# Performance work log

Measured on AMD Instinct MI355X. Metric: run time of the kernel, lower is better.

Reference implementation:

```python
import jax, jax.numpy as jnp
import numpy as np
import math

GRID_SIZE = 5
ORDER = 3
TAU = 0.1            # HuxleyRD tau (constructor default)
Q_SCALE = 64 / 2.0   # SaturatedQuantizer levels=64


def make_grid():
    h = 2.0 / GRID_SIZE
    # knots: arange(-order, grid_size+order+1)*h - 1  -> 12 values, shared by all in_features
    return jnp.arange(-ORDER, GRID_SIZE + ORDER + 1, dtype=jnp.float32) * h - 1.0


def b_splines(x, grid):
    # x: [b, in] -> bases: [b, in, GRID_SIZE+ORDER] via vectorized Cox-de Boor
    xg = x[..., None]
    g = grid  # [12], identical per feature so plain broadcasting suffices
    bases = ((xg >= g[:-1]) & (xg < g[1:])).astype(x.dtype)  # [b, in, 11]
    for p in range(1, ORDER + 1):
        t_i, t_ip = g[:-1 - p], g[p:-1]
        term1 = (xg - t_i) / (t_ip - t_i + 1e-8) * bases[..., :-1]
        t_i1, t_ip1 = g[1:-p], g[p + 1:]
        term2 = (t_ip1 - xg) / (t_ip1 - t_i1 + 1e-8) * bases[..., 1:]
        bases = term1 + term2
    return bases  # [b, in, 8]


def kan_layer(x, base_w, spline_w, grid):
    base = x @ base_w.T
    basis = b_splines(x, grid)
    # SaturatedQuantizer forward (round to levels); STE expressed via stop_gradient
    qw = spline_w + jax.lax.stop_gradient(jnp.round(spline_w * Q_SCALE) / Q_SCALE - spline_w)
    return base + jnp.einsum('bic,oic->bo', basis, qw)


def trig_unfolding(u, gcve_pressure, chirality, tau_decay):
    # u: [b, n]
    tr_c = jnp.sum(u * u, axis=-1)                                   # [b]
    uf_abs = jnp.abs(jnp.fft.rfft(u, axis=-1))                       # [b, n//2+1]
    det_pas = jnp.var(uf_abs, axis=-1, ddof=1) + 1e-6                # torch.var is unbiased
    denom = 2.0 * jnp.sqrt(det_pas) ** 3 + 1e-8
    cos_3phi = jnp.clip((3.0 * gcve_pressure - tr_c / tau_decay) / denom, -0.999, 0.999)
    phi = jnp.arccos(cos_3phi) / 3.0                                 # [b]
    lam_min = jnp.min(uf_abs, axis=-1)                               # [b]
    amp = 2.0 * jnp.sqrt(lam_min / 3.0 + 1e-8)                       # [b]
    ks = jnp.arange(3, dtype=u.dtype)                                # branch indices 0,1,2
    cos_terms = jnp.cos(phi[None, :] + 2.0 * jnp.pi * ks[:, None] / 3.0)   # [3, b]
    shifts = jnp.exp(-jnp.abs(chirality)[None, :] * ks[:, None])           # [3, b]
    coef = amp[None, :] * cos_terms * shifts                                # [3, b]
    branches = coef[:, :, None] * u[None, :, :]                             # [3, b, n]
    energies = jnp.linalg.norm(branches, axis=-1)                           # [3, b]
    best_k = jnp.argmax(energies, axis=0)                                   # [b]
    mask = (best_k[None, :] == jnp.arange(3)[:, None]).astype(u.dtype)      # [3, b]
    return jnp.sum(branches * mask[:, :, None], axis=0)


def huxley_rd(u, spectral_gate, kernel, a, gamma, tau_decay, soliton_velocity,
              gcve_pressure, chirality):
    N = u.shape[-1]
    # HarmonicWaveDecomposition: spectral sigmoid gate split
    uf = jnp.fft.rfft(u, axis=-1)
    gate = jax.nn.sigmoid(spectral_gate)
    u_erg = jnp.fft.irfft(uf * gate, n=N, axis=-1)
    u_ne = jnp.fft.irfft(uf * (1.0 - gate), n=N, axis=-1)
    # ergodic: cubic reaction + 3-tap diffusion conv (padding=1, cross-correlation)
    reaction = u_erg * (u_erg - a) * (1.0 - u_erg)
    up = jnp.pad(u_erg, ((0, 0), (1, 1)))
    diffusion = kernel[0] * up[:, :-2] + kernel[1] * up[:, 1:-1] + kernel[2] * up[:, 2:]
    u_erg_next = u_erg + TAU * (reaction + gamma * diffusion)
    # non-ergodic: spectral phase shift (soliton translation)
    nef = jnp.fft.rfft(u_ne, axis=-1)
    k_idx = jnp.arange(nef.shape[-1], dtype=jnp.float32)
    phase = jnp.exp(-1j * 2.0 * jnp.pi * k_idx * soliton_velocity / N)
    u_ne_shift = jnp.fft.irfft(nef * phase, n=N, axis=-1)
    u_ne_unf = trig_unfolding(u_ne_shift, gcve_pressure, chirality, tau_decay)
    s = u_erg_next + u_ne_unf
    return jax.nn.sigmoid(s) * s  # SiLU-style fusion


def setup_inputs() -> dict:
    key = jax.random.key(0)
    ks = jax.random.split(key, 12)
    B, NIN, W, NOUT = 4096, 512, 1024, 1024
    return {
        'c': jax.random.uniform(ks[0], (B, NIN), jnp.float32, -1.0, 1.0),
        'base_w0': jax.random.normal(ks[1], (W, NIN), jnp.float32) * (1.0 / np.sqrt(NIN)),
        'spline_w0': jax.random.normal(ks[2], (W, NIN, 8), jnp.float32) * 0.1,
        'base_w1': jax.random.normal(ks[3], (W, W), jnp.float32) * (1.0 / np.sqrt(W)),
        'spline_w1': jax.random.normal(ks[4], (W, W, 8), jnp.float32) * 0.1,
        'base_w2': jax.random.normal(ks[5], (NOUT, W), jnp.float32) * (1.0 / np.sqrt(W)),
        'spline_w2': jax.random.normal(ks[6], (NOUT, W, 8), jnp.float32) * 0.1,
        'spectral_gate': jnp.ones((NOUT // 2 + 1,), jnp.float32),
        'diffusion_kernel': jnp.asarray([0.1, -0.2, 0.1], jnp.float32),
        'a_param': jnp.asarray(0.1, jnp.float32),
        'gamma': jnp.asarray(1.0, jnp.float32),
        'tau_decay': jnp.asarray(0.1, jnp.float32),
        'soliton_velocity': jnp.asarray(0.25, jnp.float32),
        'gcve_pressure': jax.random.uniform(ks[7], (B,), jnp.float32),
        'chirality': jax.random.normal(ks[8], (B,), jnp.float32),
    }


def reference(c, base_w0, spline_w0, base_w1, spline_w1, base_w2, spline_w2,
              spectral_gate, diffusion_kernel, a_param, gamma, tau_decay,
              soliton_velocity, gcve_pressure, chirality):
    grid = make_grid()
    x = kan_layer(c, base_w0, spline_w0, grid)
    x = kan_layer(x, base_w1, spline_w1, grid)
    x = kan_layer(x, base_w2, spline_w2, grid)
    return huxley_rd(x, spectral_gate, diffusion_kernel, a_param, gamma,
                     tau_decay, soliton_velocity, gcve_pressure, chirality)
```

## Files before the change

kernel.cpp:

```cpp
#include <hip/hip_runtime.h>
#include <math.h>

typedef _Float16 f16;
typedef _Float16 f16x8 __attribute__((ext_vector_type(8)));
typedef float f32x4 __attribute__((ext_vector_type(4)));

__global__ __launch_bounds__(256) void expand_sum_a(
    const float* __restrict__ src, size_t plane, int Sin,
    f16* __restrict__ Aexp, int KIN, int shift)
{
    int idx = blockIdx.x * 256 + threadIdx.x;
    int i = idx & (KIN - 1);
    int b = idx >> shift;
    float x = 0.0f;
    for (int s = 0; s < Sin; ++s) x += src[(size_t)s * plane + idx];

    float xs = (x + 2.2f) * 2.5f;
    float fj = floorf(xs);
    int jj = (int)fj;
    float t = xs - fj;
    float t2 = t * t, t3 = t2 * t;
    float omt = 1.0f - t;
    float p0 = omt * omt * omt * (1.0f / 6.0f);
    float p1 = (3.0f * t3 - 6.0f * t2 + 4.0f) * (1.0f / 6.0f);
    float p2 = (-3.0f * t3 + 3.0f * t2 + 3.0f * t + 1.0f) * (1.0f / 6.0f);
    float p3 = t3 * (1.0f / 6.0f);

    union { f16 h[8]; uint4 v; } hi, lo;
    bool inr = (jj >= 0 && jj <= 10);
    #pragma unroll
    for (int cc = 0; cc < 8; ++cc) {
        int d = cc - (jj - 3);
        float v = 0.0f;
        if (inr) {
            if (d == 0) v = p0; else if (d == 1) v = p1;
            else if (d == 2) v = p2; else if (d == 3) v = p3;
        }
        f16 h = (f16)v;
        hi.h[cc] = h;
        lo.h[cc] = (f16)(v - (float)h);
    }
    size_t KEXP = (size_t)KIN * 19;
    f16* row = Aexp + (size_t)b * KEXP;
    *(uint4*)(row + (size_t)i * 8) = hi.v;
    *(uint4*)(row + (size_t)KIN * 8 + (size_t)i * 8) = lo.v;
    f16 xh = (f16)x;
    f16 xl = (f16)(x - (float)xh);
    int K16 = KIN * 16;
    row[K16 + i] = xh;
    row[K16 + KIN + i] = xh;
    row[K16 + 2 * KIN + i] = xl;
}

__global__ __launch_bounds__(256) void prep_b(
    const float* __restrict__ BW, const float* __restrict__ SW,
    f16* __restrict__ Bexp, int KIN, int shift)
{
    int idx = blockIdx.x * 256 + threadIdx.x;
    int i = idx & (KIN - 1);
    int o = idx >> shift;
    const float* sp = SW + ((size_t)o * KIN + i) * 8;
    union { f16 h[8]; uint4 v; } pk;
    #pragma unroll
    for (int cc = 0; cc < 8; ++cc)
        pk.h[cc] = (f16)(rintf(sp[cc] * 32.0f) * 0.03125f);
    size_t KEXP = (size_t)KIN * 19;
    f16* row = Bexp + (size_t)o * KEXP;
    *(uint4*)(row + (size_t)i * 8) = pk.v;
    *(uint4*)(row + (size_t)KIN * 8 + (size_t)i * 8) = pk.v;
    float w = BW[(size_t)o * KIN + i];
    f16 wh = (f16)w;
    f16 wl = (f16)(w - (float)wh);
    int K16 = KIN * 16;
    row[K16 + i] = wh;
    row[K16 + KIN + i] = wl;
    row[K16 + 2 * KIN + i] = wh;
}

__global__ __launch_bounds__(512, 2) void gemm_mfma(
    const f16* __restrict__ A, const f16* __restrict__ Bm,
    float* __restrict__ C, int Kfull, int Kc, size_t plane, int N)
{
    __shared__ __align__(16) f16 As[4][8192];
    __shared__ __align__(16) f16 Bs[4][8192];

    const int tid = threadIdx.x;
    const int wave = tid >> 6, lane = tid & 63;

    const int nwg = gridDim.x * gridDim.y * gridDim.z;
    const int b = blockIdx.x + gridDim.x * (blockIdx.y + gridDim.y * blockIdx.z);
    const int q = nwg >> 3;
    const int L = (b & 7) * q + (b >> 3);
    const int lx = L % gridDim.x;
    const int rest = L / gridDim.x;
    const int ly = rest % gridDim.y;
    const int lz = rest / gridDim.y;

    const int m0 = ly * 256, n0 = lx * 256;
    const int kb = lz * Kc;
    int kcl = Kfull - kb; if (kcl > Kc) kcl = Kc;
    const int NT = kcl >> 5;

    const int kc_src = (lane & 3) ^ ((lane >> 3) & 3);
    const f16* gb[4];
    int isA_[4], coff[4];
    #pragma unroll
    for (int j = 0; j < 4; ++j) {
        int cch = wave * 4 + j;
        int a = (cch < 16);
        int c8 = a ? cch : (cch - 16);
        int row0 = (a ? m0 : n0) + c8 * 16 + (lane >> 2);
        gb[j] = (a ? A : Bm) + (size_t)row0 * Kfull + kb + kc_src * 8;
        isA_[j] = a;
        coff[j] = c8 * 512;
    }

    f32x4 acc[8][4];
    #pragma unroll
    for (int i = 0; i < 8; ++i)
        #pragma unroll
        for (int j = 0; j < 4; ++j)
            acc[i][j] = (f32x4){0.f, 0.f, 0.f, 0.f};

    #pragma unroll
    for (int s = 0; s < 3; ++s) {
        if (s < NT) {
            int k0 = s << 5;
            #pragma unroll
            for (int j = 0; j < 4; ++j) {
                f16* dp = isA_[j] ? &As[s][coff[j]] : &Bs[s][coff[j]];
                __builtin_amdgcn_global_load_lds(
                    (const __attribute__((address_space(1))) unsigned int*)(gb[j] + k0),
                    (__attribute__((address_space(3))) unsigned int*)dp, 16, 0, 0);
            }
        }
    }
    if (NT >= 3)      asm volatile("s_waitcnt vmcnt(8)" ::: "memory");
    else if (NT == 2) asm volatile("s_waitcnt vmcnt(4)" ::: "memory");
    else              asm volatile("s_waitcnt vmcnt(0)" ::: "memory");
    __builtin_amdgcn_s_barrier();
    asm volatile("" ::: "memory");

    const int lr = lane & 15;
    const int ko = (((lane >> 4) ^ ((lr >> 1) & 3)) & 3) * 8;
    const int wm = (wave & 1) * 128, wn = (wave >> 1) * 64;

    for (int t = 0; t < NT; ++t) {
        const int st = t & 3;
        const int ns = (t + 3) & 3;
        const bool pf = (t + 3 < NT);
        const int kn = (t + 3) << 5;
        const int rem = NT - 1 - t;

        f16x8 af[4], bf[4], ag[4];
        #pragma unroll
        for (int i = 0; i < 4; ++i)
            af[i] = *(const f16x8*)&As[st][(wm + i * 16 + lr) * 32 + ko];
        #pragma unroll
        for (int j = 0; j < 4; ++j)
            bf[j] = *(const f16x8*)&Bs[st][(wn + j * 16 + lr) * 32 + ko];
        __builtin_amdgcn_sched_barrier(0);
        #pragma unroll
        for (int i = 0; i < 4; ++i)
            ag[i] = *(const f16x8*)&As[st][(wm + 64 + i * 16 + lr) * 32 + ko];
        __builtin_amdgcn_sched_barrier(0);

        if (rem >= 2)      asm volatile("s_waitcnt vmcnt(4)" ::: "memory");
        else if (rem == 1) asm volatile("s_waitcnt vmcnt(0)" ::: "memory");
        if (rem >= 1) {
            __builtin_amdgcn_s_barrier();
            asm volatile("" ::: "memory");
        }

        if (pf) {
            #pragma unroll
            for (int j = 0; j < 4; ++j) {
                f16* dp = isA_[j] ? &As[ns][coff[j]] : &Bs[ns][coff[j]];
                __builtin_amdgcn_global_load_lds(
                    (const __attribute__((address_space(1))) unsigned int*)(gb[j] + kn),
                    (__attribute__((address_space(3))) unsigned int*)dp, 16, 0, 0);
            }
        }

        asm volatile("s_waitcnt lgkmcnt(4)" ::: "memory");
        __builtin_amdgcn_sched_barrier(0);
        __builtin_amdgcn_s_setprio(1);
        #pragma unroll
        for (int i = 0; i < 4; ++i)
            #pragma unroll
            for (int j = 0; j < 4; ++j)
                acc[i][j] = __builtin_amdgcn_mfma_f32_16x16x32_f16(af[i], bf[j], acc[i][j], 0, 0, 0);
        __builtin_amdgcn_s_setprio(0);

        asm volatile("s_waitcnt lgkmcnt(0)" ::: "memory");
        __builtin_amdgcn_sched_barrier(0);
        __builtin_amdgcn_s_setprio(1);
        #pragma unroll
        for (int i = 0; i < 4; ++i)
            #pragma unroll
            for (int j = 0; j < 4; ++j)
                acc[4 + i][j] = __builtin_amdgcn_mfma_f32_16x16x32_f16(ag[i], bf[j], acc[4 + i][j], 0, 0, 0);
        __builtin_amdgcn_s_setprio(0);
    }

    float* Cp = C + (size_t)lz * plane;
    #pragma unroll
    for (int i = 0; i < 8; ++i) {
        int row = m0 + wm + i * 16 + (lane >> 4) * 4;
        #pragma unroll
        for (int j = 0; j < 4; ++j) {
            int col = n0 + wn + j * 16 + lr;
            #pragma unroll
            for (int rr = 0; rr < 4; ++rr)
                Cp[(size_t)(row + rr) * N + col] = acc[i][j][rr];
        }
    }
}

__global__ __launch_bounds__(256) void kan_gemm(
    const float* __restrict__ X, const float* __restrict__ BW,
    const float* __restrict__ SW, float* __restrict__ Y, int KIN, int OUT)
{
    __shared__ __align__(16) float Asf[72][68];
    __shared__ __align__(16) float Bsf[72][68];
    const int tid = threadIdx.x;
    const int n0 = blockIdx.x * 64;
    const int m0 = blockIdx.y * 64;
    const int tx = tid & 15;
    const int ty = tid >> 4;
    float acc[4][4] = {};
    for (int k0 = 0; k0 < KIN; k0 += 8) {
        #pragma unroll
        for (int rep = 0; rep < 2; ++rep) {
            int idx = rep * 256 + tid;
            int r = idx >> 3, c = idx & 7;
            float x = X[(size_t)(m0 + r) * KIN + k0 + c];
            int bk = c * 9;
            Asf[bk][r] = x;
            #pragma unroll
            for (int z = 0; z < 8; ++z) Asf[bk + 1 + z][r] = 0.0f;
            float xs = (x + 2.2f) * 2.5f;
            float fj = floorf(xs);
            int j = (int)fj;
            if (j >= 0 && j <= 10) {
                float t = xs - fj;
                float t2 = t * t, t3 = t2 * t;
                float omt = 1.0f - t;
                float p0 = omt * omt * omt * (1.0f / 6.0f);
                float p1 = (3.0f * t3 - 6.0f * t2 + 4.0f) * (1.0f / 6.0f);
                float p2 = (-3.0f * t3 + 3.0f * t2 + 3.0f * t + 1.0f) * (1.0f / 6.0f);
                float p3 = t3 * (1.0f / 6.0f);
                if (j >= 3) Asf[bk + 1 + j - 3][r] = p0;
                if (j >= 2 && j <= 9) Asf[bk + 1 + j - 2][r] = p1;
                if (j >= 1 && j <= 8) Asf[bk + 1 + j - 1][r] = p2;
                if (j <= 7) Asf[bk + 1 + j][r] = p3;
            }
        }
        #pragma unroll
        for (int rep = 0; rep < 16; ++rep) {
            int idx = rep * 256 + tid;
            int ol = idx >> 6;
            int l = idx & 63;
            int i = l >> 3, cc = l & 7;
            float v = SW[((size_t)(n0 + ol) * KIN + k0 + i) * 8 + cc];
            Bsf[i * 9 + 1 + cc][ol] = rintf(v * 32.0f) * 0.03125f;
        }
        #pragma unroll
        for (int rep = 0; rep < 2; ++rep) {
            int idx = rep * 256 + tid;
            int ol = idx >> 3, cc = idx & 7;
            Bsf[cc * 9][ol] = BW[(size_t)(n0 + ol) * KIN + k0 + cc];
        }
        __syncthreads();
        #pragma unroll 8
        for (int kk = 0; kk < 72; ++kk) {
            float4 av = *(const float4*)&Asf[kk][ty * 4];
            float4 bv = *(const float4*)&Bsf[kk][tx * 4];
            acc[0][0] += av.x * bv.x; acc[0][1] += av.x * bv.y; acc[0][2] += av.x * bv.z; acc[0][3] += av.x * bv.w;
            acc[1][0] += av.y * bv.x; acc[1][1] += av.y * bv.y; acc[1][2] += av.y * bv.z; acc[1][3] += av.y * bv.w;
            acc[2][0] += av.z * bv.x; acc[2][1] += av.z * bv.y; acc[2][2] += av.z * bv.z; acc[2][3] += av.z * bv.w;
            acc[3][0] += av.w * bv.x; acc[3][1] += av.w * bv.y; acc[3][2] += av.w * bv.z; acc[3][3] += av.w * bv.w;
        }
        __syncthreads();
    }
    #pragma unroll
    for (int i = 0; i < 4; ++i) {
        float4 o = make_float4(acc[i][0], acc[i][1], acc[i][2], acc[i][3]);
        *(float4*)&Y[(size_t)(m0 + ty * 4 + i) * OUT + n0 + tx * 4] = o;
    }
}

__device__ __forceinline__ float block_reduce_sum(float v, float* red, int tid) {
    red[tid] = v; __syncthreads();
    #pragma unroll
    for (int s = 128; s > 0; s >>= 1) {
        if (tid < s) red[tid] += red[tid + s];
        __syncthreads();
    }
    float r = red[0]; __syncthreads();
    return r;
}
__device__ __forceinline__ float block_reduce_min(float v, float* red, int tid) {
    red[tid] = v; __syncthreads();
    #pragma unroll
    for (int s = 128; s > 0; s >>= 1) {
        if (tid < s) red[tid] = fminf(red[tid], red[tid + s]);
        __syncthreads();
    }
    float r = red[0]; __syncthreads();
    return r;
}

__device__ void fft1024(float2* X, const float2* tw, int tid, bool inverse) {
    if (!inverse) {
        for (int sh = 9; sh >= 0; --sh) {
            int h = 1 << sh;
            #pragma unroll
            for (int q = 0; q < 2; ++q) {
                int b = tid + q * 256;
                int g = b >> sh, j = b & (h - 1);
                int i0 = (g << (sh + 1)) + j, i1 = i0 + h;
                float2 u = X[i0], v = X[i1];
                float dx = u.x - v.x, dy = u.y - v.y;
                X[i0] = make_float2(u.x + v.x, u.y + v.y);
                float2 w = tw[j << (9 - sh)];
                X[i1] = make_float2(dx * w.x + dy * w.y, dy * w.x - dx * w.y);
            }
            __syncthreads();
        }
    } else {
        for (int sh = 0; sh <= 9; ++sh) {
            int h = 1 << sh;
            #pragma unroll
            for (int q = 0; q < 2; ++q) {
                int b = tid + q * 256;
                int g = b >> sh, j = b & (h - 1);
                int i0 = (g << (sh + 1)) + j, i1 = i0 + h;
                float2 u = X[i0], v = X[i1];
                float2 w = tw[j << (9 - sh)];
                float tx2 = v.x * w.x - v.y * w.y;
                float ty2 = v.x * w.y + v.y * w.x;
                X[i0] = make_float2(u.x + tx2, u.y + ty2);
                X[i1] = make_float2(u.x - tx2, u.y - ty2);
            }
            __syncthreads();
        }
    }
}

__global__ __launch_bounds__(256) void huxley_kernel(
    const float* __restrict__ Pin, size_t plane, int S,
    float* __restrict__ dst,
    const float* __restrict__ sg, const float* __restrict__ dk,
    const float* __restrict__ pa, const float* __restrict__ pgam,
    const float* __restrict__ ptau, const float* __restrict__ pvel,
    const float* __restrict__ gp, const float* __restrict__ chi)
{
    __shared__ float2 A[1024];
    __shared__ float2 Bb[1024];
    __shared__ float sErg[1024];
    __shared__ float sAbs[516];
    __shared__ float2 tw[512];
    __shared__ float red[256];
    __shared__ float sG[516];

    const int tid = threadIdx.x;
    const int row = blockIdx.x;
    const float* pin = Pin + (size_t)row * 1024;
    float* uo = dst + (size_t)row * 1024;

    for (int m = tid; m < 512; m += 256) {
        float s, c;
        sincosf(6.283185307179586f * (float)m * (1.0f / 1024.0f), &s, &c);
        tw[m] = make_float2(c, s);
    }
    for (int k = tid; k < 513; k += 256)
        sG[k] = 1.0f / (1.0f + expf(-sg[k]));
    for (int i = tid; i < 1024; i += 256) {
        float s = 0.0f;
        for (int ss = 0; ss < S; ++ss) s += pin[(size_t)ss * plane + i];
        A[i] = make_float2(s, 0.0f);
    }
    __syncthreads();

    fft1024(A, tw, tid, false);

    for (int p = tid; p < 1024; p += 256) {
        int k = (int)(__brev((unsigned)p) >> 22);
        int m = (k <= 512) ? k : 1024 - k;
        float g = sG[m] * (1.0f / 1024.0f);
        Bb[p] = make_float2(A[p].x * g, A[p].y * g);
    }
    __syncthreads();
    fft1024(Bb, tw, tid, true);
    for (int i = tid; i < 1024; i += 256) sErg[i] = Bb[i].x;
    __syncthreads();

    const float vv = pvel[0];
    for (int p = tid; p < 1024; p += 256) {
        int k = (int)(__brev((unsigned)p) >> 22);
        int m = (k <= 512) ? k : 1024 - k;
        float omg = 1.0f - sG[m];
        float nx = A[p].x * omg, ny = A[p].y * omg;
        float ang = (k <= 512)
            ? (-6.283185307179586f * vv * (float)k * (1.0f / 1024.0f))
            : (6.283185307179586f * vv * (float)(1024 - k) * (1.0f / 1024.0f));
        float sn, cs;
        sincosf(ang, &sn, &cs);
        float yx = nx * cs - ny * sn;
        float yy = nx * sn + ny * cs;
        if (k < 512)       sAbs[k]   = sqrtf(nx * nx + ny * ny);
        else if (k == 512) sAbs[512] = fabsf(yx);
        Bb[p] = make_float2(yx * (1.0f / 1024.0f), yy * (1.0f / 1024.0f));
    }
    __syncthreads();
    fft1024(Bb, tw, tid, true);

    float loc = 0.0f;
    for (int i = tid; i < 1024; i += 256) { float x = Bb[i].x; loc += x * x; }
    float trc = block_reduce_sum(loc, red, tid);

    loc = 0.0f;
    for (int k = tid; k < 513; k += 256) loc += sAbs[k];
    float mean = block_reduce_sum(loc, red, tid) * (1.0f / 513.0f);

    loc = 0.0f;
    for (int k = tid; k < 513; k += 256) { float d = sAbs[k] - mean; loc += d * d; }
    float varsum = block_reduce_sum(loc, red, tid);

    loc = 3.4e38f;
    for (int k = tid; k < 513; k += 256) loc = fminf(loc, sAbs[k]);
    float lmin = block_reduce_min(loc, red, tid);

    float det_pas = varsum * (1.0f / 512.0f) + 1e-6f;
    float sd = sqrtf(det_pas);
    float denom = 2.0f * sd * sd * sd + 1e-8f;
    float c3 = (3.0f * gp[row] - trc / ptau[0]) / denom;
    c3 = fminf(fmaxf(c3, -0.999f), 0.999f);
    float ph = acosf(c3) * (1.0f / 3.0f);
    float amp = 2.0f * sqrtf(lmin * (1.0f / 3.0f) + 1e-8f);
    float nu = sqrtf(trc);
    float achi = fabsf(chi[row]);
    float cbest = 0.0f, ebest = -1.0f;
    #pragma unroll
    for (int kb = 0; kb < 3; ++kb) {
        float ck = amp * cosf(ph + 2.0943951023931953f * (float)kb) * expf(-achi * (float)kb);
        float ek = fabsf(ck) * nu;
        if (ek > ebest) { ebest = ek; cbest = ck; }
    }

    const float a = pa[0], gm = pgam[0];
    const float k0 = dk[0], k1 = dk[1], k2 = dk[2];
    for (int i = tid; i < 1024; i += 256) {
        float e = sErg[i];
        float l = (i > 0) ? sErg[i - 1] : 0.0f;
        float r = (i < 1023) ? sErg[i + 1] : 0.0f;
        float reac = e * (e - a) * (1.0f - e);
        float diff = k0 * l + k1 * e + k2 * r;
        float un = e + 0.1f * (reac + gm * diff);
        float s = un + cbest * Bb[i].x;
        uo[i] = s / (1.0f + expf(-s));
    }
}


extern "C" void kernel_launch(void* const* d_in, const int* in_sizes, int n_in,
                              void* d_out, int out_size, void* d_ws, size_t ws_size,
                              hipStream_t stream) {
    const float* c    = (const float*)d_in[0];
    const float* bw0  = (const float*)d_in[1];
    const float* sw0  = (const float*)d_in[2];
    const float* bw1  = (const float*)d_in[3];
    const float* sw1  = (const float*)d_in[4];
    const float* bw2  = (const float*)d_in[5];
    const float* sw2  = (const float*)d_in[6];
    const float* sg   = (const float*)d_in[7];
    const float* dk   = (const float*)d_in[8];
    const float* pa   = (const float*)d_in[9];
    const float* pgam = (const float*)d_in[10];
    const float* ptau = (const float*)d_in[11];
    const float* pvel = (const float*)d_in[12];
    const float* gp   = (const float*)d_in[13];
    const float* chi  = (const float*)d_in[14];

    const int B = 4096, NIN = 512, W = 1024, NOUT = 1024;
    const int KE0 = 19 * NIN, KE1 = 19 * W;
    const size_t MN = (size_t)B * W;
    const size_t BE = (size_t)W * KE1 * 2;
    dim3 blk(256);
    dim3 gblk(512);

    struct Cand { int CH, S; };
    const Cand cands[] = {
        {4096, 4}, {4096, 3}, {2048, 4}, {2048, 3}, {1024, 4},
        {512, 4}, {256, 4}
    };
    int CH = 0, S = 1;
    for (const auto& cd : cands) {
        size_t need = BE + (size_t)cd.CH * KE1 * 2 + (size_t)cd.S * MN * 4;
        if (need <= ws_size) { CH = cd.CH; S = cd.S; break; }
    }

    if (CH > 0) {
        f16* Bexp = (f16*)d_ws;
        float* P  = (float*)((char*)d_ws + BE);
        f16* Aexp = (f16*)((char*)d_ws + BE + (size_t)S * MN * 4);

        const int Kc0 = ((KE0 / 32 + S - 1) / S) * 32;
        const int Kc1 = ((KE1 / 32 + S - 1) / S) * 32;

        prep_b<<<(W * NIN) / 256, blk, 0, stream>>>(bw0, sw0, Bexp, NIN, 9);
        for (int r0 = 0; r0 < B; r0 += CH) {
            expand_sum_a<<<(CH * NIN) / 256, blk, 0, stream>>>(
                c + (size_t)r0 * NIN, 0, 1, Aexp, NIN, 9);
            gemm_mfma<<<dim3(W / 256, CH / 256, S), gblk, 0, stream>>>(
                Aexp, Bexp, P + (size_t)r0 * W, KE0, Kc0, MN, W);
        }
        prep_b<<<(W * W) / 256, blk, 0, stream>>>(bw1, sw1, Bexp, W, 10);
        for (int r0 = 0; r0 < B; r0 += CH) {
            expand_sum_a<<<(CH * W) / 256, blk, 0, stream>>>(
                P + (size_t)r0 * W, MN, S, Aexp, W, 10);
            gemm_mfma<<<dim3(W / 256, CH / 256, S), gblk, 0, stream>>>(
                Aexp, Bexp, P + (size_t)r0 * W, KE1, Kc1, MN, W);
        }
        prep_b<<<(NOUT * W) / 256, blk, 0, stream>>>(bw2, sw2, Bexp, W, 10);
        for (int r0 = 0; r0 < B; r0 += CH) {
            expand_sum_a<<<(CH * W) / 256, blk, 0, stream>>>(
                P + (size_t)r0 * W, MN, S, Aexp, W, 10);
            gemm_mfma<<<dim3(NOUT / 256, CH / 256, S), gblk, 0, stream>>>(
                Aexp, Bexp, P + (size_t)r0 * W, KE1, Kc1, MN, NOUT);
        }
        huxley_kernel<<<B, blk, 0, stream>>>(P, MN, S, (float*)d_out,
                                             sg, dk, pa, pgam, ptau, pvel, gp, chi);
    } else {
        float* fx0 = (float*)d_ws;
        float* fx1 = fx0 + (size_t)B * W;
        dim3 g0(W / 64, B / 64);
        kan_gemm<<<g0, blk, 0, stream>>>(c,   bw0, sw0, fx0, NIN, W);
        kan_gemm<<<g0, blk, 0, stream>>>(fx0, bw1, sw1, fx1, W,   W);
        dim3 g2(NOUT / 64, B / 64);
        kan_gemm<<<g2, blk, 0, stream>>>(fx1, bw2, sw2, (float*)d_out, W, NOUT);
        huxley_kernel<<<B, blk, 0, stream>>>((float*)d_out, 0, 1, (float*)d_out,
                                             sg, dk, pa, pgam, ptau, pvel, gp, chi);
    }
}
```

Before: 698.5 us.

## Switch MFMA GEMM to 64-wide K tiles with double-buffered LDS pipeline

Changes the GEMM main loop from a 4-stage ring of 32-wide K tiles to a 2-stage double buffer of 64-wide K tiles, with a new 8-way XOR swizzle. LDS fragment reads for the second K half are interleaved with the MFMAs of the first half, and the global-to-LDS prefetch is split in two halves. The aim is to halve the number of barriers per unit of K and overlap LDS reads with MFMA work. In exchange the prefetch distance drops to one stage, so global latency is less hidden, and the K-split chunk sizes must now be multiples of 64.

After: 690.8 us. Within noise of the previous version (-1.1%).

```diff
diff --git a/kernel.cpp b/kernel.cpp
--- a/kernel.cpp
+++ b/kernel.cpp
@@ -81,8 +81,8 @@
     const f16* __restrict__ A, const f16* __restrict__ Bm,
     float* __restrict__ C, int Kfull, int Kc, size_t plane, int N)
 {
-    __shared__ __align__(16) f16 As[4][8192];
-    __shared__ __align__(16) f16 Bs[4][8192];
+    __shared__ __align__(16) f16 As[2][16384];
+    __shared__ __align__(16) f16 Bs[2][16384];
 
     const int tid = threadIdx.x;
     const int wave = tid >> 6, lane = tid & 63;
@@ -99,17 +99,17 @@
     const int m0 = ly * 256, n0 = lx * 256;
     const int kb = lz * Kc;
     int kcl = Kfull - kb; if (kcl > Kc) kcl = Kc;
-    const int NT = kcl >> 5;
-
-    const int kc_src = (lane & 3) ^ ((lane >> 3) & 3);
-    const f16* gb[4];
-    int isA_[4], coff[4];
-    #pragma unroll
-    for (int j = 0; j < 4; ++j) {
-        int cch = wave * 4 + j;
-        int a = (cch < 16);
-        int c8 = a ? cch : (cch - 16);
-        int row0 = (a ? m0 : n0) + c8 * 16 + (lane >> 2);
+    const int NT = kcl >> 6;
+
+    const int kc_src = (lane & 7) ^ ((lane >> 3) & 7);
+    const f16* gb[8];
+    int isA_[8], coff[8];
+    #pragma unroll
+    for (int j = 0; j < 8; ++j) {
+        int cch = wave * 8 + j;
+        int a = (cch < 32);
+        int c8 = a ? cch : (cch - 32);
+        int row0 = (a ? m0 : n0) + c8 * 8 + (lane >> 3);
         gb[j] = (a ? A : Bm) + (size_t)row0 * Kfull + kb + kc_src * 8;
         isA_[j] = a;
         coff[j] = c8 * 512;
@@ -123,61 +123,47 @@
             acc[i][j] = (f32x4){0.f, 0.f, 0.f, 0.f};
 
     #pragma unroll
-    for (int s = 0; s < 3; ++s) {
-        if (s < NT) {
-            int k0 = s << 5;
-            #pragma unroll
-            for (int j = 0; j < 4; ++j) {
-                f16* dp = isA_[j] ? &As[s][coff[j]] : &Bs[s][coff[j]];
-                __builtin_amdgcn_global_load_lds(
-                    (const __attribute__((address_space(1))) unsigned int*)(gb[j] + k0),
-                    (__attribute__((address_space(3))) unsigned int*)dp, 16, 0, 0);
-            }
-        }
-    }
-    if (NT >= 3)      asm volatile("s_waitcnt vmcnt(8)" ::: "memory");
-    else if (NT == 2) asm volatile("s_waitcnt vmcnt(4)" ::: "memory");
-    else              asm volatile("s_waitcnt vmcnt(0)" ::: "memory");
+    for (int j = 0; j < 8; ++j) {
+        f16* dp = isA_[j] ? &As[0][coff[j]] : &Bs[0][coff[j]];
+        __builtin_amdgcn_global_load_lds(
+            (const __attribute__((address_space(1))) unsigned int*)(gb[j]),
+            (__attribute__((address_space(3))) unsigned int*)dp, 16, 0, 0);
+    }
+    asm volatile("s_waitcnt vmcnt(0)" ::: "memory");
     __builtin_amdgcn_s_barrier();
     asm volatile("" ::: "memory");
 
     const int lr = lane & 15;
-    const int ko = (((lane >> 4) ^ ((lr >> 1) & 3)) & 3) * 8;
+    const int g4 = lane >> 4;
+    const int ko0 = ((g4     ^ (lr & 7))) * 8;
+    const int ko1 = (((4|g4) ^ (lr & 7))) * 8;
     const int wm = (wave & 1) * 128, wn = (wave >> 1) * 64;
 
     for (int t = 0; t < NT; ++t) {
-        const int st = t & 3;
-        const int ns = (t + 3) & 3;
-        const bool pf = (t + 3 < NT);
-        const int kn = (t + 3) << 5;
-        const int rem = NT - 1 - t;
-
-        f16x8 af[4], bf[4], ag[4];
-        #pragma unroll
-        for (int i = 0; i < 4; ++i)
-            af[i] = *(const f16x8*)&As[st][(wm + i * 16 + lr) * 32 + ko];
+        const int st = t & 1;
+        const int ns = st ^ 1;
+        const bool pf = (t + 1 < NT);
+        const int kt = (t + 1) << 6;
+
+        f16x8 af0[4], bf0[4], ag0[4], af1[4], bf1[4], ag1[4];
+
+        #pragma unroll
+        for (int i = 0; i < 4; ++i)
+            af0[i] = *(const f16x8*)&As[st][(wm + i * 16 + lr) * 64 + ko0];
         #pragma unroll
         for (int j = 0; j < 4; ++j)
-            bf[j] = *(const f16x8*)&Bs[st][(wn + j * 16 + lr) * 32 + ko];
-        __builtin_amdgcn_sched_barrier(0);
-        #pragma unroll
-        for (int i = 0; i < 4; ++i)
-            ag[i] = *(const f16x8*)&As[st][(wm + 64 + i * 16 + lr) * 32 + ko];
-        __builtin_amdgcn_sched_barrier(0);
-
-        if (rem >= 2)      asm volatile("s_waitcnt vmcnt(4)" ::: "memory");
-        else if (rem == 1) asm volatile("s_waitcnt vmcnt(0)" ::: "memory");
-        if (rem >= 1) {
-            __builtin_amdgcn_s_barrier();
-            asm volatile("" ::: "memory");
-        }
-
+            bf0[j] = *(const f16x8*)&Bs[st][(wn + j * 16 + lr) * 64 + ko0];
+        __builtin_amdgcn_sched_barrier(0);
+        #pragma unroll
+        for (int i = 0; i < 4; ++i)
+            ag0[i] = *(const f16x8*)&As[st][(wm + 64 + i * 16 + lr) * 64 + ko0];
+        __builtin_amdgcn_sched_barrier(0);
         if (pf) {
             #pragma unroll
             for (int j = 0; j < 4; ++j) {
                 f16* dp = isA_[j] ? &As[ns][coff[j]] : &Bs[ns][coff[j]];
                 __builtin_amdgcn_global_load_lds(
-                    (const __attribute__((address_space(1))) unsigned int*)(gb[j] + kn),
+                    (const __attribute__((address_space(1))) unsigned int*)(gb[j] + kt),
                     (__attribute__((address_space(3))) unsigned int*)dp, 16, 0, 0);
             }
         }
@@ -189,9 +175,51 @@
         for (int i = 0; i < 4; ++i)
             #pragma unroll
             for (int j = 0; j < 4; ++j)
-                acc[i][j] = __builtin_amdgcn_mfma_f32_16x16x32_f16(af[i], bf[j], acc[i][j], 0, 0, 0);
+                acc[i][j] = __builtin_amdgcn_mfma_f32_16x16x32_f16(af0[i], bf0[j], acc[i][j], 0, 0, 0);
         __builtin_amdgcn_s_setprio(0);
 
+        #pragma unroll
+        for (int i = 0; i < 4; ++i)
+            af1[i] = *(const f16x8*)&As[st][(wm + i * 16 + lr) * 64 + ko1];
+        #pragma unroll
+        for (int j = 0; j < 4; ++j)
+            bf1[j] = *(const f16x8*)&Bs[st][(wn + j * 16 + lr) * 64 + ko1];
+        __builtin_amdgcn_sched_barrier(0);
+
+        asm volatile("s_waitcnt lgkmcnt(8)" ::: "memory");
+        __builtin_amdgcn_sched_barrier(0);
+        __builtin_amdgcn_s_setprio(1);
+        #pragma unroll
+        for (int i = 0; i < 4; ++i)
+            #pragma unroll
+            for (int j = 0; j < 4; ++j)
+                acc[4 + i][j] = __builtin_amdgcn_mfma_f32_16x16x32_f16(ag0[i], bf0[j], acc[4 + i][j], 0, 0, 0);
+        __builtin_amdgcn_s_setprio(0);
+
+        #pragma unroll
+        for (int i = 0; i < 4; ++i)
+            ag1[i] = *(const f16x8*)&As[st][(wm + 64 + i * 16 + lr) * 64 + ko1];
+        __builtin_amdgcn_sched_barrier(0);
+        if (pf) {
+            #pragma unroll
+            for (int j = 4; j < 8; ++j) {
+                f16* dp = isA_[j] ? &As[ns][coff[j]] : &Bs[ns][coff[j]];
+                __builtin_amdgcn_global_load_lds(
+                    (const __attribute__((address_space(1))) unsigned int*)(gb[j] + kt),
+                    (__attribute__((address_space(3))) unsigned int*)dp, 16, 0, 0);
+            }
+        }
+
+        asm volatile("s_waitcnt lgkmcnt(4)" ::: "memory");
+        __builtin_amdgcn_sched_barrier(0);
+        __builtin_amdgcn_s_setprio(1);
+        #pragma unroll
+        for (int i = 0; i < 4; ++i)
+            #pragma unroll
+            for (int j = 0; j < 4; ++j)
+                acc[i][j] = __builtin_amdgcn_mfma_f32_16x16x32_f16(af1[i], bf1[j], acc[i][j], 0, 0, 0);
+        __builtin_amdgcn_s_setprio(0);
+
         asm volatile("s_waitcnt lgkmcnt(0)" ::: "memory");
         __builtin_amdgcn_sched_barrier(0);
         __builtin_amdgcn_s_setprio(1);
@@ -199,8 +227,15 @@
         for (int i = 0; i < 4; ++i)
             #pragma unroll
             for (int j = 0; j < 4; ++j)
-                acc[4 + i][j] = __builtin_amdgcn_mfma_f32_16x16x32_f16(ag[i], bf[j], acc[4 + i][j], 0, 0, 0);
+                acc[4 + i][j] = __builtin_amdgcn_mfma_f32_16x16x32_f16(ag1[i], bf1[j], acc[4 + i][j], 0, 0, 0);
         __builtin_amdgcn_s_setprio(0);
+
+        if (pf) {
+            asm volatile("s_waitcnt vmcnt(0)" ::: "memory");
+            __builtin_amdgcn_sched_barrier(0);
+            __builtin_amdgcn_s_barrier();
+            asm volatile("" ::: "memory");
+        }
     }
 
     float* Cp = C + (size_t)lz * plane;
@@ -506,8 +541,8 @@
         float* P  = (float*)((char*)d_ws + BE);
         f16* Aexp = (f16*)((char*)d_ws + BE + (size_t)S * MN * 4);
 
-        const int Kc0 = ((KE0 / 32 + S - 1) / S) * 32;
-        const int Kc1 = ((KE1 / 32 + S - 1) / S) * 32;
+        const int Kc0 = ((KE0 / 64 + S - 1) / S) * 64;
+        const int Kc1 = ((KE1 / 64 + S - 1) / S) * 64;
 
         prep_b<<<(W * NIN) / 256, blk, 0, stream>>>(bw0, sw0, Bexp, NIN, 9);
         for (int r0 = 0; r0 < B; r0 += CH) {
```
